# Kernel tuning notes

Hardware: AMD Instinct MI355X
Metric: run time of the kernel (lower is better)

Reference implementation:

```python
import jax, jax.numpy as jnp
import numpy as np

B, S, HID, NH = 2, 2048, 1024, 16
HD = HID // NH
NEG = -1e10


def setup_inputs() -> dict:
    key = jax.random.key(0)
    ks = jax.random.split(key, 14)
    s = 0.02
    return {
        "query": jax.random.normal(ks[0], (B, S, HID), jnp.float32),
        "key_": jax.random.normal(ks[1], (B, S, HID), jnp.float32),
        "value": jax.random.normal(ks[2], (B, S, HID), jnp.float32),
        "mask": jax.random.randint(ks[3], (B, 1, 1, S), 0, 2, jnp.int32),
        "Wq": jax.random.normal(ks[4], (HID, HID), jnp.float32) * s,
        "bq": jnp.zeros((HID,), jnp.float32),
        "Wk": jax.random.normal(ks[5], (HID, HID), jnp.float32) * s,
        "bk": jnp.zeros((HID,), jnp.float32),
        "Wv": jax.random.normal(ks[6], (HID, HID), jnp.float32) * s,
        "bv": jnp.zeros((HID,), jnp.float32),
        "Ww": jax.random.normal(ks[7], (HD, HD), jnp.float32) * s,
        "bw": jnp.zeros((HD,), jnp.float32),
        "Wo": jax.random.normal(ks[8], (HID, HID), jnp.float32) * s,
        "bo": jnp.zeros((HID,), jnp.float32),
    }


def reference(query, key_, value, mask, Wq, bq, Wk, bk, Wv, bv, Ww, bw, Wo, bo):
    def heads(x, W, b):
        h = x @ W.T + b                       # [B,S,HID]
        return h.reshape(B, S, NH, HD).transpose(0, 2, 1, 3)  # [B,H,S,D]

    Q = heads(query, Wq, bq)
    K = heads(key_, Wk, bk)
    V = heads(value, Wv, bv)
    # multiplicative: per-head linear on Q before QK^T (no 1/sqrt(d) scale)
    Qw = Q @ Ww.T + bw                        # [B,H,S,D]
    energy = jnp.einsum('bhqd,bhkd->bhqk', Qw, K)
    energy = jnp.where(mask == 0, jnp.float32(NEG), energy)
    attention = jax.nn.softmax(energy, axis=-1)
    x = jnp.einsum('bhqk,bhkd->bhqd', attention, V)  # dropout p=0 (eval)
    x = x.transpose(0, 2, 1, 3).reshape(B, S, HID)
    x = x @ Wo.T + bo
    return (x, attention)
```

## Files before the change

kernel.cpp:

```cpp
#include <hip/hip_runtime.h>
#include <hip/hip_bf16.h>

#define B_    2
#define S_    2048
#define HID_  1024
#define NH_   16
#define HD_   64
#define M_    (B_ * S_)
#define NEGB_ (-1.0e30f)
#define LOG2E 1.44269504088896340736f
#define X_ELEMS 4194304

typedef __bf16 bf16;
typedef bf16  bf16x2 __attribute__((ext_vector_type(2)));
typedef bf16  bf16x4 __attribute__((ext_vector_type(4)));
typedef bf16  bf16x8 __attribute__((ext_vector_type(8)));
typedef float f32x4  __attribute__((ext_vector_type(4)));

static __device__ __forceinline__ f32x4 mfma16(bf16x8 a, bf16x8 b, f32x4 c) {
    return __builtin_amdgcn_mfma_f32_16x16x32_bf16(a, b, c, 0, 0, 0);
}

static __device__ __forceinline__ int pack2(float x, float y) {
    union { bf16x2 h; int i; } u;
    u.h = bf16x2{(bf16)x, (bf16)y};
    return u.i;
}

static __device__ __forceinline__ int swadr(int row, int chunk) {
    return row * 128 + ((chunk ^ (row & 7)) << 4);
}
static __device__ __forceinline__ bf16x8 lds8(const bf16* base, int row, int chunk) {
    return *(const bf16x8*)((const char*)base + swadr(row, chunk));
}


__global__ void cast3(const float* __restrict__ a, const float* __restrict__ b,
                      const float* __restrict__ c, bf16* __restrict__ oa,
                      bf16* __restrict__ ob, bf16* __restrict__ oc) {
    const float* in = blockIdx.y == 0 ? a : blockIdx.y == 1 ? b : c;
    bf16* out = blockIdx.y == 0 ? oa : blockIdx.y == 1 ? ob : oc;
    int i = (blockIdx.x * 256 + threadIdx.x) * 4;
    float4 v = *(const float4*)(in + i);
    out[i + 0] = (bf16)v.x;
    out[i + 1] = (bf16)v.y;
    out[i + 2] = (bf16)v.z;
    out[i + 3] = (bf16)v.w;
}

__global__ __launch_bounds__(256) void fuse_wq(const float* __restrict__ Ww,
                                               const float* __restrict__ Wq,
                                               const float* __restrict__ bq,
                                               const float* __restrict__ bw,
                                               bf16* __restrict__ Wq_eff,
                                               float* __restrict__ bq_eff) {
    __shared__ float ww[64][64];
    const int h = blockIdx.x >> 2, chunk = blockIdx.x & 3;
    const int i = chunk * 256 + threadIdx.x;
    for (int t = threadIdx.x; t < 4096; t += 256) ww[t >> 6][t & 63] = Ww[t];
    __syncthreads();
    float col[64];
    #pragma unroll
    for (int d = 0; d < 64; ++d) col[d] = Wq[(size_t)(h * 64 + d) * 1024 + i];
    for (int j = 0; j < 64; ++j) {
        float acc = 0.f;
        #pragma unroll
        for (int d = 0; d < 64; ++d) acc += ww[j][d] * col[d];
        Wq_eff[(size_t)(h * 64 + j) * 1024 + i] = (bf16)(acc * LOG2E);
    }
    if (chunk == 0 && threadIdx.x < 64) {
        int j = threadIdx.x;
        float acc = bw[j];
        for (int d = 0; d < 64; ++d) acc += ww[j][d] * bq[h * 64 + d];
        bq_eff[h * 64 + j] = acc * LOG2E;
    }
}

__global__ __launch_bounds__(256, 3) void proj3(const float* __restrict__ Aq,
                                                const float* __restrict__ Ak,
                                                const float* __restrict__ Av,
                                                const bf16* __restrict__ W0,
                                                const bf16* __restrict__ W1,
                                                const bf16* __restrict__ W2,
                                                const float* __restrict__ b0,
                                                const float* __restrict__ b1,
                                                const float* __restrict__ b2,
                                                bf16* __restrict__ Qw,
                                                bf16* __restrict__ Kh,
                                                bf16* __restrict__ Vt) {
    __shared__ __align__(16) bf16 Ast[2][128 * 64];
    __shared__ __align__(16) bf16 Wst[2][64 * 64];
    const int z = blockIdx.z;
    const float* A = z == 0 ? Aq : z == 1 ? Ak : Av;
    const bf16* W = z == 0 ? W0 : z == 1 ? W1 : W2;
    const float* bias = z == 0 ? b0 : z == 1 ? b1 : b2;

    const int tid = threadIdx.x;
    const int wave = tid >> 6, lane = tid & 63;
    const int lr = lane & 15, kg = lane >> 4;
    const int mb0 = blockIdx.x * 128;
    const int n0 = blockIdx.y * 64;

    const int arow = tid >> 1, akc = (tid & 1) * 32;
    const int wrow = tid >> 2, wkc = (tid & 3) * 16;

    float4 ar[8];
    bf16x8 wr[2];
    auto loadT = [&](int k0) {
        const float4* ap = (const float4*)(A + (size_t)(mb0 + arow) * HID_ + k0 + akc);
        #pragma unroll
        for (int j = 0; j < 8; ++j) ar[j] = ap[j];
        const bf16* wp = W + (size_t)(n0 + wrow) * HID_ + k0 + wkc;
        wr[0] = *(const bf16x8*)wp;
        wr[1] = *(const bf16x8*)(wp + 8);
    };
    auto writeT = [&](int buf) {
        #pragma unroll
        for (int c = 0; c < 4; ++c) {
            float4 x0 = ar[2 * c], x1 = ar[2 * c + 1];
            bf16x8 v;
            v[0] = (bf16)x0.x; v[1] = (bf16)x0.y; v[2] = (bf16)x0.z; v[3] = (bf16)x0.w;
            v[4] = (bf16)x1.x; v[5] = (bf16)x1.y; v[6] = (bf16)x1.z; v[7] = (bf16)x1.w;
            *(bf16x8*)((char*)Ast[buf] + swadr(arow, (akc >> 3) + c)) = v;
        }
        *(bf16x8*)((char*)Wst[buf] + swadr(wrow, wkc >> 3)) = wr[0];
        *(bf16x8*)((char*)Wst[buf] + swadr(wrow, (wkc >> 3) + 1)) = wr[1];
    };

    f32x4 acc[2][4] = {};
    loadT(0);
    for (int t = 0; t < 16; ++t) {
        const int buf = t & 1;
        writeT(buf);
        if (t < 15) loadT((t + 1) * 64);
        __syncthreads();
        const bf16* ab = Ast[buf];
        const bf16* wb = Wst[buf];
        #pragma unroll
        for (int kp = 0; kp < 2; ++kp) {
            bf16x8 af0 = lds8(ab, wave * 16 + lr, kp * 4 + kg);
            bf16x8 af1 = lds8(ab, 64 + wave * 16 + lr, kp * 4 + kg);
            #pragma unroll
            for (int nf = 0; nf < 4; ++nf) {
                bf16x8 wf = lds8(wb, nf * 16 + lr, kp * 4 + kg);
                acc[0][nf] = mfma16(af0, wf, acc[0][nf]);
                acc[1][nf] = mfma16(af1, wf, acc[1][nf]);
            }
        }
        __syncthreads();
    }

    const int m_base = mb0 + wave * 16;
    #pragma unroll
    for (int t = 0; t < 2; ++t) {
        #pragma unroll
        for (int cg = 0; cg < 4; ++cg) {
            int col = n0 + cg * 16 + lr;
            float bv = bias[col];
            int h = col >> 6, d = col & 63;
            #pragma unroll
            for (int r = 0; r < 4; ++r) {
                int m = m_base + t * 64 + kg * 4 + r;
                int b = m >> 11, s = m & 2047;
                float val = acc[t][cg][r] + bv;
                if (z == 0)
                    Qw[((size_t)(b * NH_ + h) * S_ + s) * HD_ + d] = (bf16)val;
                else if (z == 1)
                    Kh[((size_t)(b * NH_ + h) * S_ + s) * HD_ + d] = (bf16)val;
                else
                    Vt[((size_t)(b * NH_ + h) * HD_ + d) * S_ + s] = (bf16)val;
            }
        }
    }
}

__global__ __launch_bounds__(512, 4) void attn_kernel(const bf16* __restrict__ Qw,
                                                      const bf16* __restrict__ Kh,
                                                      const bf16* __restrict__ Vt,
                                                      const int* __restrict__ mask,
                                                      float* __restrict__ attn_out,
                                                      bf16* __restrict__ Xh) {
    __shared__ __align__(16) float negf[S_];
    __shared__ __align__(16) bf16 Kst[2][4096];
    __shared__ __align__(16) bf16 Vst[2][4096];

    const int lane = threadIdx.x & 63, wave = threadIdx.x >> 6;
    const int lr = lane & 15, kg = lane >> 4;

    const int wg = blockIdx.x;
    const int flat = (wg & 7) * 64 + (wg >> 3);
    const int qtile = flat & 15;
    const int bh = flat >> 4;
    const int b = bh >> 4, h = bh & 15;
    const int q0 = qtile * 128 + wave * 16;

    const bf16* Qh = Qw + (size_t)bh * S_ * HD_;
    const bf16* Kb = Kh + (size_t)bh * S_ * HD_;
    const bf16* Vb = Vt + (size_t)bh * HD_ * S_;
    const int*  mb = mask + b * S_;
    float* arow = attn_out + (size_t)bh * S_ * S_;

    for (int t = threadIdx.x; t < S_; t += 512)
        negf[t] = mb[t] ? 0.f : NEGB_;

    const int srow = threadIdx.x >> 3;
    const int sch  = threadIdx.x & 7;
    const int sdst = srow * 128 + ((sch ^ (srow & 7)) << 4);

    bf16x8 a0 = *(const bf16x8*)(Qh + (size_t)(q0 + lr) * HD_ + kg * 8);
    bf16x8 a1 = *(const bf16x8*)(Qh + (size_t)(q0 + lr) * HD_ + 32 + kg * 8);

    const int addrA = (lr + (((kg << 1)    ) & 3) * 16) << 2;
    const int addrB = (lr + (((kg << 1) | 1) & 3) * 16) << 2;
    const bool lt2 = kg < 2;

    __syncthreads();

    bf16x8 kreg = *(const bf16x8*)(Kb + (size_t)srow * HD_ + sch * 8);
    bf16x8 vreg = *(const bf16x8*)(Vb + (size_t)srow * S_ + sch * 8);

    float psum = 0.f;
    f32x4 X[4] = {};
    for (int t = 0; t < 32; ++t) {
        const int buf = t & 1;
        *(bf16x8*)((char*)Kst[buf] + sdst) = kreg;
        *(bf16x8*)((char*)Vst[buf] + sdst) = vreg;
        if (t + 1 < 32) {
            kreg = *(const bf16x8*)(Kb + (size_t)((t + 1) * 64 + srow) * HD_ + sch * 8);
            vreg = *(const bf16x8*)(Vb + (size_t)srow * S_ + (t + 1) * 64 + sch * 8);
        }
        __syncthreads();
        const bf16* kb = Kst[buf];
        const bf16* vb = Vst[buf];
        #pragma unroll
        for (int s2 = 0; s2 < 2; ++s2) {
            const int rlo = s2 * 32 + lr, rhi = s2 * 32 + 16 + lr;
            bf16x8 k0a = lds8(kb, rlo, kg);
            bf16x8 k1a = lds8(kb, rlo, 4 + kg);
            bf16x8 k0b = lds8(kb, rhi, kg);
            bf16x8 k1b = lds8(kb, rhi, 4 + kg);
            f32x4 e0 = *(const f32x4*)&negf[t * 64 + s2 * 32 + kg * 4];
            f32x4 e1 = *(const f32x4*)&negf[t * 64 + s2 * 32 + 16 + kg * 4];
            e0 = mfma16(k0a, a0, e0);
            e0 = mfma16(k1a, a1, e0);
            e1 = mfma16(k0b, a0, e1);
            e1 = mfma16(k1b, a1, e1);
            f32x4 p0, p1;
            #pragma unroll
            for (int r = 0; r < 4; ++r) { p0[r] = exp2f(e0[r]); p1[r] = exp2f(e1[r]); }
            psum += (p0[0] + p0[1] + p0[2] + p0[3]) + (p1[0] + p1[1] + p1[2] + p1[3]);
            int q0d = pack2(p0[0], p0[1]);
            int q1d = pack2(p0[2], p0[3]);
            int q2d = pack2(p1[0], p1[1]);
            int q3d = pack2(p1[2], p1[3]);
            int bA0 = __builtin_amdgcn_ds_bpermute(addrA, q0d);
            int bA1 = __builtin_amdgcn_ds_bpermute(addrA, q1d);
            int bA2 = __builtin_amdgcn_ds_bpermute(addrA, q2d);
            int bA3 = __builtin_amdgcn_ds_bpermute(addrA, q3d);
            int bB0 = __builtin_amdgcn_ds_bpermute(addrB, q0d);
            int bB1 = __builtin_amdgcn_ds_bpermute(addrB, q1d);
            int bB2 = __builtin_amdgcn_ds_bpermute(addrB, q2d);
            int bB3 = __builtin_amdgcn_ds_bpermute(addrB, q3d);
            union { int d[4]; bf16x8 v; } pau;
            pau.d[0] = lt2 ? bA0 : bA2;
            pau.d[1] = lt2 ? bA1 : bA3;
            pau.d[2] = lt2 ? bB0 : bB2;
            pau.d[3] = lt2 ? bB1 : bB3;
            #pragma unroll
            for (int ds = 0; ds < 4; ++ds) {
                bf16x8 v = lds8(vb, ds * 16 + lr, s2 * 4 + kg);
                X[ds] = mfma16(v, pau.v, X[ds]);
            }
        }
    }

    psum += __shfl_xor(psum, 16);
    psum += __shfl_xor(psum, 32);
    const float lg2l = __log2f(psum);
    const float linv = 1.0f / psum;

    {
        bf16* xrow = Xh + ((size_t)(b * S_ + q0 + lr)) * HID_ + h * HD_;
        #pragma unroll
        for (int ds = 0; ds < 4; ++ds) {
            bf16x4 xv;
            #pragma unroll
            for (int r = 0; r < 4; ++r) xv[r] = (bf16)(X[ds][r] * linv);
            *(bf16x4*)(xrow + ds * 16 + kg * 4) = xv;
        }
    }

    kreg = *(const bf16x8*)(Kb + (size_t)srow * HD_ + sch * 8);
    for (int t = 0; t < 32; ++t) {
        const int buf = t & 1;
        *(bf16x8*)((char*)Kst[buf] + sdst) = kreg;
        if (t + 1 < 32)
            kreg = *(const bf16x8*)(Kb + (size_t)((t + 1) * 64 + srow) * HD_ + sch * 8);
        __syncthreads();
        const bf16* kb = Kst[buf];
        #pragma unroll
        for (int j = 0; j < 4; ++j) {
            const int row = j * 16 + lr;
            bf16x8 k0 = lds8(kb, row, kg);
            bf16x8 k1 = lds8(kb, row, 4 + kg);
            f32x4 z = *(const f32x4*)&negf[t * 64 + j * 16 + kg * 4];
            z[0] -= lg2l; z[1] -= lg2l; z[2] -= lg2l; z[3] -= lg2l;
            z = mfma16(k0, a0, z);
            z = mfma16(k1, a1, z);
            f32x4 p;
            #pragma unroll
            for (int r = 0; r < 4; ++r) p[r] = exp2f(z[r]);
            *(f32x4*)(arow + (size_t)(q0 + lr) * S_ + t * 64 + j * 16 + kg * 4) = p;
        }
    }
}

__global__ __launch_bounds__(256, 3) void out_gemm(const bf16* __restrict__ X,
                                                   const bf16* __restrict__ Wo,
                                                   const float* __restrict__ bo,
                                                   float* __restrict__ out) {
    __shared__ __align__(16) bf16 Ast[2][128 * 64];
    __shared__ __align__(16) bf16 Wst[2][64 * 64];

    const int tid = threadIdx.x;
    const int wave = tid >> 6, lane = tid & 63;
    const int lr = lane & 15, kg = lane >> 4;
    const int mb0 = blockIdx.x * 128;
    const int n0 = blockIdx.y * 64;

    const int arow = tid >> 1, akc = (tid & 1) * 32;
    const int wrow = tid >> 2, wkc = (tid & 3) * 16;

    bf16x8 ar[4];
    bf16x8 wr[2];
    auto loadT = [&](int k0) {
        const bf16* ap = X + (size_t)(mb0 + arow) * HID_ + k0 + akc;
        #pragma unroll
        for (int j = 0; j < 4; ++j) ar[j] = *(const bf16x8*)(ap + j * 8);
        const bf16* wp = Wo + (size_t)(n0 + wrow) * HID_ + k0 + wkc;
        wr[0] = *(const bf16x8*)wp;
        wr[1] = *(const bf16x8*)(wp + 8);
    };
    auto writeT = [&](int buf) {
        #pragma unroll
        for (int c = 0; c < 4; ++c)
            *(bf16x8*)((char*)Ast[buf] + swadr(arow, (akc >> 3) + c)) = ar[c];
        *(bf16x8*)((char*)Wst[buf] + swadr(wrow, wkc >> 3)) = wr[0];
        *(bf16x8*)((char*)Wst[buf] + swadr(wrow, (wkc >> 3) + 1)) = wr[1];
    };

    f32x4 acc[2][4] = {};
    loadT(0);
    for (int t = 0; t < 16; ++t) {
        const int buf = t & 1;
        writeT(buf);
        if (t < 15) loadT((t + 1) * 64);
        __syncthreads();
        const bf16* ab = Ast[buf];
        const bf16* wb = Wst[buf];
        #pragma unroll
        for (int kp = 0; kp < 2; ++kp) {
            bf16x8 af0 = lds8(ab, wave * 16 + lr, kp * 4 + kg);
            bf16x8 af1 = lds8(ab, 64 + wave * 16 + lr, kp * 4 + kg);
            #pragma unroll
            for (int nf = 0; nf < 4; ++nf) {
                bf16x8 wf = lds8(wb, nf * 16 + lr, kp * 4 + kg);
                acc[0][nf] = mfma16(af0, wf, acc[0][nf]);
                acc[1][nf] = mfma16(af1, wf, acc[1][nf]);
            }
        }
        __syncthreads();
    }

    const int m_base = mb0 + wave * 16;
    #pragma unroll
    for (int t = 0; t < 2; ++t) {
        #pragma unroll
        for (int cg = 0; cg < 4; ++cg) {
            int col = n0 + cg * 16 + lr;
            float bv = bo[col];
            #pragma unroll
            for (int r = 0; r < 4; ++r)
                out[(size_t)(m_base + t * 64 + kg * 4 + r) * HID_ + col] = acc[t][cg][r] + bv;
        }
    }
}

extern "C" void kernel_launch(void* const* d_in, const int* in_sizes, int n_in,
                              void* d_out, int out_size, void* d_ws, size_t ws_size,
                              hipStream_t stream) {
    const float* query = (const float*)d_in[0];
    const float* key_  = (const float*)d_in[1];
    const float* value = (const float*)d_in[2];
    const int*   mask  = (const int*)d_in[3];
    const float* Wq = (const float*)d_in[4];
    const float* bq = (const float*)d_in[5];
    const float* Wk = (const float*)d_in[6];
    const float* bk = (const float*)d_in[7];
    const float* Wv = (const float*)d_in[8];
    const float* bv = (const float*)d_in[9];
    const float* Ww = (const float*)d_in[10];
    const float* bw = (const float*)d_in[11];
    const float* Wo = (const float*)d_in[12];
    const float* bo = (const float*)d_in[13];
    float* out = (float*)d_out;

    char* ws = (char*)d_ws;
    size_t off = 0;
    auto alloc = [&](size_t bytes) {
        void* p = ws + off;
        off += (bytes + 255) & ~(size_t)255;
        return p;
    };
    bf16*  Wq_eff = (bf16*)alloc((size_t)HID_ * HID_ * 2);
    float* bq_eff = (float*)alloc((size_t)HID_ * 4);
    bf16*  Wk_b   = (bf16*)alloc((size_t)HID_ * HID_ * 2);
    bf16*  Wv_b   = (bf16*)alloc((size_t)HID_ * HID_ * 2);
    bf16*  Wo_b   = (bf16*)alloc((size_t)HID_ * HID_ * 2);
    bf16*  Qw     = (bf16*)alloc((size_t)M_ * HID_ * 2);
    bf16*  Kh     = (bf16*)alloc((size_t)M_ * HID_ * 2);
    bf16*  Vt     = (bf16*)alloc((size_t)M_ * HID_ * 2);
    bf16*  Xh     = (bf16*)alloc((size_t)M_ * HID_ * 2);
    (void)ws_size; (void)in_sizes; (void)n_in; (void)out_size;

    dim3 gcast(1024, 3);
    cast3<<<gcast, 256, 0, stream>>>(Wk, Wv, Wo, Wk_b, Wv_b, Wo_b);
    fuse_wq<<<64, 256, 0, stream>>>(Ww, Wq, bq, bw, Wq_eff, bq_eff);

    dim3 gproj(M_ / 128, HID_ / 64, 3);
    proj3<<<gproj, 256, 0, stream>>>(query, key_, value,
                                     Wq_eff, Wk_b, Wv_b,
                                     bq_eff, bk, bv,
                                     Qw, Kh, Vt);

    attn_kernel<<<512, 512, 0, stream>>>(Qw, Kh, Vt, mask, out + X_ELEMS, Xh);

    dim3 gout(M_ / 128, HID_ / 64);
    out_gemm<<<gout, 256, 0, stream>>>(Xh, Wo_b, bo, out);
}
```

Measured before the change: 364.0 us.

## Process two query tiles per wave to reuse K/V fragments, halve block size

Each wave now computes 32 query rows (two 16-row sets) instead of 16, reusing the K and V fragments loaded from LDS for both sets. The block shrinks to 256 threads covering the same 128 query rows, with each thread staging two 16-byte chunks per tile. This cuts LDS reads and barrier cost per MFMA but doubles accumulator registers and reduces wave count, which could lower latency hiding.

```diff
diff --git a/kernel.cpp b/kernel.cpp
--- a/kernel.cpp
+++ b/kernel.cpp
@@ -174,7 +174,7 @@
     }
 }
 
-__global__ __launch_bounds__(512, 4) void attn_kernel(const bf16* __restrict__ Qw,
+__global__ __launch_bounds__(256, 3) void attn_kernel(const bf16* __restrict__ Qw,
                                                       const bf16* __restrict__ Kh,
                                                       const bf16* __restrict__ Vt,
                                                       const int* __restrict__ mask,
@@ -184,7 +184,8 @@
     __shared__ __align__(16) bf16 Kst[2][4096];
     __shared__ __align__(16) bf16 Vst[2][4096];
 
-    const int lane = threadIdx.x & 63, wave = threadIdx.x >> 6;
+    const int tid = threadIdx.x;
+    const int lane = tid & 63, wave = tid >> 6;
     const int lr = lane & 15, kg = lane >> 4;
 
     const int wg = blockIdx.x;
@@ -192,7 +193,7 @@
     const int qtile = flat & 15;
     const int bh = flat >> 4;
     const int b = bh >> 4, h = bh & 15;
-    const int q0 = qtile * 128 + wave * 16;
+    const int q0 = qtile * 128 + wave * 32;
 
     const bf16* Qh = Qw + (size_t)bh * S_ * HD_;
     const bf16* Kb = Kh + (size_t)bh * S_ * HD_;
@@ -200,15 +201,18 @@
     const int*  mb = mask + b * S_;
     float* arow = attn_out + (size_t)bh * S_ * S_;
 
-    for (int t = threadIdx.x; t < S_; t += 512)
+    for (int t = tid; t < S_; t += 256)
         negf[t] = mb[t] ? 0.f : NEGB_;
 
-    const int srow = threadIdx.x >> 3;
-    const int sch  = threadIdx.x & 7;
-    const int sdst = srow * 128 + ((sch ^ (srow & 7)) << 4);
-
-    bf16x8 a0 = *(const bf16x8*)(Qh + (size_t)(q0 + lr) * HD_ + kg * 8);
-    bf16x8 a1 = *(const bf16x8*)(Qh + (size_t)(q0 + lr) * HD_ + 32 + kg * 8);
+    const int srow = tid >> 2;
+    const int sc0  = tid & 3;
+
+    bf16x8 aQ[2][2];
+    #pragma unroll
+    for (int set = 0; set < 2; ++set) {
+        aQ[set][0] = *(const bf16x8*)(Qh + (size_t)(q0 + set * 16 + lr) * HD_ + kg * 8);
+        aQ[set][1] = *(const bf16x8*)(Qh + (size_t)(q0 + set * 16 + lr) * HD_ + 32 + kg * 8);
+    }
 
     const int addrA = (lr + (((kg << 1)    ) & 3) * 16) << 2;
     const int addrB = (lr + (((kg << 1) | 1) & 3) * 16) << 2;
@@ -216,86 +220,114 @@
 
     __syncthreads();
 
-    bf16x8 kreg = *(const bf16x8*)(Kb + (size_t)srow * HD_ + sch * 8);
-    bf16x8 vreg = *(const bf16x8*)(Vb + (size_t)srow * S_ + sch * 8);
-
-    float psum = 0.f;
-    f32x4 X[4] = {};
+    bf16x8 kreg[2], vreg[2];
+    #pragma unroll
+    for (int j = 0; j < 2; ++j) {
+        kreg[j] = *(const bf16x8*)(Kb + (size_t)srow * HD_ + (sc0 + 4 * j) * 8);
+        vreg[j] = *(const bf16x8*)(Vb + (size_t)srow * S_ + (sc0 + 4 * j) * 8);
+    }
+
+    float psum[2] = {0.f, 0.f};
+    f32x4 X[2][4] = {};
     for (int t = 0; t < 32; ++t) {
         const int buf = t & 1;
-        *(bf16x8*)((char*)Kst[buf] + sdst) = kreg;
-        *(bf16x8*)((char*)Vst[buf] + sdst) = vreg;
+        #pragma unroll
+        for (int j = 0; j < 2; ++j) {
+            *(bf16x8*)((char*)Kst[buf] + swadr(srow, sc0 + 4 * j)) = kreg[j];
+            *(bf16x8*)((char*)Vst[buf] + swadr(srow, sc0 + 4 * j)) = vreg[j];
+        }
         if (t + 1 < 32) {
-            kreg = *(const bf16x8*)(Kb + (size_t)((t + 1) * 64 + srow) * HD_ + sch * 8);
-            vreg = *(const bf16x8*)(Vb + (size_t)srow * S_ + (t + 1) * 64 + sch * 8);
+            #pragma unroll
+            for (int j = 0; j < 2; ++j) {
+                kreg[j] = *(const bf16x8*)(Kb + (size_t)((t + 1) * 64 + srow) * HD_ + (sc0 + 4 * j) * 8);
+                vreg[j] = *(const bf16x8*)(Vb + (size_t)srow * S_ + (t + 1) * 64 + (sc0 + 4 * j) * 8);
+            }
         }
         __syncthreads();
         const bf16* kb = Kst[buf];
         const bf16* vb = Vst[buf];
         #pragma unroll
         for (int s2 = 0; s2 < 2; ++s2) {
-            const int rlo = s2 * 32 + lr, rhi = s2 * 32 + 16 + lr;
-            bf16x8 k0a = lds8(kb, rlo, kg);
-            bf16x8 k1a = lds8(kb, rlo, 4 + kg);
-            bf16x8 k0b = lds8(kb, rhi, kg);
-            bf16x8 k1b = lds8(kb, rhi, 4 + kg);
-            f32x4 e0 = *(const f32x4*)&negf[t * 64 + s2 * 32 + kg * 4];
-            f32x4 e1 = *(const f32x4*)&negf[t * 64 + s2 * 32 + 16 + kg * 4];
-            e0 = mfma16(k0a, a0, e0);
-            e0 = mfma16(k1a, a1, e0);
-            e1 = mfma16(k0b, a0, e1);
-            e1 = mfma16(k1b, a1, e1);
-            f32x4 p0, p1;
-            #pragma unroll
-            for (int r = 0; r < 4; ++r) { p0[r] = exp2f(e0[r]); p1[r] = exp2f(e1[r]); }
-            psum += (p0[0] + p0[1] + p0[2] + p0[3]) + (p1[0] + p1[1] + p1[2] + p1[3]);
-            int q0d = pack2(p0[0], p0[1]);
-            int q1d = pack2(p0[2], p0[3]);
-            int q2d = pack2(p1[0], p1[1]);
-            int q3d = pack2(p1[2], p1[3]);
-            int bA0 = __builtin_amdgcn_ds_bpermute(addrA, q0d);
-            int bA1 = __builtin_amdgcn_ds_bpermute(addrA, q1d);
-            int bA2 = __builtin_amdgcn_ds_bpermute(addrA, q2d);
-            int bA3 = __builtin_amdgcn_ds_bpermute(addrA, q3d);
-            int bB0 = __builtin_amdgcn_ds_bpermute(addrB, q0d);
-            int bB1 = __builtin_amdgcn_ds_bpermute(addrB, q1d);
-            int bB2 = __builtin_amdgcn_ds_bpermute(addrB, q2d);
-            int bB3 = __builtin_amdgcn_ds_bpermute(addrB, q3d);
-            union { int d[4]; bf16x8 v; } pau;
-            pau.d[0] = lt2 ? bA0 : bA2;
-            pau.d[1] = lt2 ? bA1 : bA3;
-            pau.d[2] = lt2 ? bB0 : bB2;
-            pau.d[3] = lt2 ? bB1 : bB3;
-            #pragma unroll
-            for (int ds = 0; ds < 4; ++ds) {
-                bf16x8 v = lds8(vb, ds * 16 + lr, s2 * 4 + kg);
-                X[ds] = mfma16(v, pau.v, X[ds]);
-            }
-        }
-    }
-
-    psum += __shfl_xor(psum, 16);
-    psum += __shfl_xor(psum, 32);
-    const float lg2l = __log2f(psum);
-    const float linv = 1.0f / psum;
-
-    {
-        bf16* xrow = Xh + ((size_t)(b * S_ + q0 + lr)) * HID_ + h * HD_;
+            bf16x8 k0a = lds8(kb, s2 * 32 + lr, kg);
+            bf16x8 k1a = lds8(kb, s2 * 32 + lr, 4 + kg);
+            bf16x8 k0b = lds8(kb, s2 * 32 + 16 + lr, kg);
+            bf16x8 k1b = lds8(kb, s2 * 32 + 16 + lr, 4 + kg);
+            f32x4 cin0 = *(const f32x4*)&negf[t * 64 + s2 * 32 + kg * 4];
+            f32x4 cin1 = *(const f32x4*)&negf[t * 64 + s2 * 32 + 16 + kg * 4];
+            bf16x8 vv[4];
+            #pragma unroll
+            for (int ds = 0; ds < 4; ++ds)
+                vv[ds] = lds8(vb, ds * 16 + lr, s2 * 4 + kg);
+            #pragma unroll
+            for (int set = 0; set < 2; ++set) {
+                f32x4 e0 = cin0, e1 = cin1;
+                e0 = mfma16(k0a, aQ[set][0], e0);
+                e0 = mfma16(k1a, aQ[set][1], e0);
+                e1 = mfma16(k0b, aQ[set][0], e1);
+                e1 = mfma16(k1b, aQ[set][1], e1);
+                f32x4 p0, p1;
+                #pragma unroll
+                for (int r = 0; r < 4; ++r) { p0[r] = exp2f(e0[r]); p1[r] = exp2f(e1[r]); }
+                psum[set] += (p0[0] + p0[1] + p0[2] + p0[3]) + (p1[0] + p1[1] + p1[2] + p1[3]);
+                int q0d = pack2(p0[0], p0[1]);
+                int q1d = pack2(p0[2], p0[3]);
+                int q2d = pack2(p1[0], p1[1]);
+                int q3d = pack2(p1[2], p1[3]);
+                int bA0 = __builtin_amdgcn_ds_bpermute(addrA, q0d);
+                int bA1 = __builtin_amdgcn_ds_bpermute(addrA, q1d);
+                int bA2 = __builtin_amdgcn_ds_bpermute(addrA, q2d);
+                int bA3 = __builtin_amdgcn_ds_bpermute(addrA, q3d);
+                int bB0 = __builtin_amdgcn_ds_bpermute(addrB, q0d);
+                int bB1 = __builtin_amdgcn_ds_bpermute(addrB, q1d);
+                int bB2 = __builtin_amdgcn_ds_bpermute(addrB, q2d);
+                int bB3 = __builtin_amdgcn_ds_bpermute(addrB, q3d);
+                union { int d[4]; bf16x8 v; } pau;
+                pau.d[0] = lt2 ? bA0 : bA2;
+                pau.d[1] = lt2 ? bA1 : bA3;
+                pau.d[2] = lt2 ? bB0 : bB2;
+                pau.d[3] = lt2 ? bB1 : bB3;
+                #pragma unroll
+                for (int ds = 0; ds < 4; ++ds)
+                    X[set][ds] = mfma16(vv[ds], pau.v, X[set][ds]);
+            }
+        }
+    }
+
+    float lg2l[2], linv[2];
+    #pragma unroll
+    for (int set = 0; set < 2; ++set) {
+        float s = psum[set];
+        s += __shfl_xor(s, 16);
+        s += __shfl_xor(s, 32);
+        lg2l[set] = __log2f(s);
+        linv[set] = 1.0f / s;
+    }
+
+    #pragma unroll
+    for (int set = 0; set < 2; ++set) {
+        bf16* xrow = Xh + ((size_t)(b * S_ + q0 + set * 16 + lr)) * HID_ + h * HD_;
         #pragma unroll
         for (int ds = 0; ds < 4; ++ds) {
             bf16x4 xv;
             #pragma unroll
-            for (int r = 0; r < 4; ++r) xv[r] = (bf16)(X[ds][r] * linv);
+            for (int r = 0; r < 4; ++r) xv[r] = (bf16)(X[set][ds][r] * linv[set]);
             *(bf16x4*)(xrow + ds * 16 + kg * 4) = xv;
         }
     }
 
-    kreg = *(const bf16x8*)(Kb + (size_t)srow * HD_ + sch * 8);
+    #pragma unroll
+    for (int j = 0; j < 2; ++j)
+        kreg[j] = *(const bf16x8*)(Kb + (size_t)srow * HD_ + (sc0 + 4 * j) * 8);
     for (int t = 0; t < 32; ++t) {
         const int buf = t & 1;
-        *(bf16x8*)((char*)Kst[buf] + sdst) = kreg;
-        if (t + 1 < 32)
-            kreg = *(const bf16x8*)(Kb + (size_t)((t + 1) * 64 + srow) * HD_ + sch * 8);
+        #pragma unroll
+        for (int j = 0; j < 2; ++j)
+            *(bf16x8*)((char*)Kst[buf] + swadr(srow, sc0 + 4 * j)) = kreg[j];
+        if (t + 1 < 32) {
+            #pragma unroll
+            for (int j = 0; j < 2; ++j)
+                kreg[j] = *(const bf16x8*)(Kb + (size_t)((t + 1) * 64 + srow) * HD_ + (sc0 + 4 * j) * 8);
+        }
         __syncthreads();
         const bf16* kb = Kst[buf];
         #pragma unroll
@@ -303,14 +335,19 @@
             const int row = j * 16 + lr;
             bf16x8 k0 = lds8(kb, row, kg);
             bf16x8 k1 = lds8(kb, row, 4 + kg);
-            f32x4 z = *(const f32x4*)&negf[t * 64 + j * 16 + kg * 4];
-            z[0] -= lg2l; z[1] -= lg2l; z[2] -= lg2l; z[3] -= lg2l;
-            z = mfma16(k0, a0, z);
-            z = mfma16(k1, a1, z);
-            f32x4 p;
-            #pragma unroll
-            for (int r = 0; r < 4; ++r) p[r] = exp2f(z[r]);
-            *(f32x4*)(arow + (size_t)(q0 + lr) * S_ + t * 64 + j * 16 + kg * 4) = p;
+            f32x4 nb = *(const f32x4*)&negf[t * 64 + j * 16 + kg * 4];
+            #pragma unroll
+            for (int set = 0; set < 2; ++set) {
+                f32x4 z;
+                #pragma unroll
+                for (int r = 0; r < 4; ++r) z[r] = nb[r] - lg2l[set];
+                z = mfma16(k0, aQ[set][0], z);
+                z = mfma16(k1, aQ[set][1], z);
+                f32x4 p;
+                #pragma unroll
+                for (int r = 0; r < 4; ++r) p[r] = exp2f(z[r]);
+                *(f32x4*)(arow + (size_t)(q0 + set * 16 + lr) * S_ + t * 64 + j * 16 + kg * 4) = p;
+            }
         }
     }
 }
@@ -433,7 +470,7 @@
                                      bq_eff, bk, bv,
                                      Qw, Kh, Vt);
 
-    attn_kernel<<<512, 512, 0, stream>>>(Qw, Kh, Vt, mask, out + X_ELEMS, Xh);
+    attn_kernel<<<512, 256, 0, stream>>>(Qw, Kh, Vt, mask, out + X_ELEMS, Xh);
 
     dim3 gout(M_ / 128, HID_ / 64);
     out_gemm<<<gout, 256, 0, stream>>>(Xh, Wo_b, bo, out);
```

Measured after the change: 366.2 us. About the same (+0.6%).

## Split attention into stats and probability-stream kernels; widen projection N tile

Applied to the files above, without the earlier changes.

The fused attention kernel is split into two launches. The first computes softmax row sums and the PV output and writes the sums to a global buffer. The second recomputes QK^T and streams the normalized probabilities to the attention output. Both use 256-thread blocks over 64-query tiles, so there are 1024 blocks each. Separately, the projection GEMM tile grows from 64 to 128 output columns with occupancy 2, which adds reuse of the A tile at the cost of more registers and LDS. The split trades an extra kernel launch and re-reading Q/K against better overlap and occupancy in each phase.

```diff
diff --git a/kernel.cpp b/kernel.cpp
--- a/kernel.cpp
+++ b/kernel.cpp
@@ -76,7 +76,7 @@
     }
 }
 
-__global__ __launch_bounds__(256, 3) void proj3(const float* __restrict__ Aq,
+__global__ __launch_bounds__(256, 2) void proj3(const float* __restrict__ Aq,
                                                 const float* __restrict__ Ak,
                                                 const float* __restrict__ Av,
                                                 const bf16* __restrict__ W0,
@@ -89,7 +89,7 @@
                                                 bf16* __restrict__ Kh,
                                                 bf16* __restrict__ Vt) {
     __shared__ __align__(16) bf16 Ast[2][128 * 64];
-    __shared__ __align__(16) bf16 Wst[2][64 * 64];
+    __shared__ __align__(16) bf16 Wst[2][128 * 64];
     const int z = blockIdx.z;
     const float* A = z == 0 ? Aq : z == 1 ? Ak : Av;
     const bf16* W = z == 0 ? W0 : z == 1 ? W1 : W2;
@@ -99,20 +99,20 @@
     const int wave = tid >> 6, lane = tid & 63;
     const int lr = lane & 15, kg = lane >> 4;
     const int mb0 = blockIdx.x * 128;
-    const int n0 = blockIdx.y * 64;
+    const int n0 = blockIdx.y * 128;
 
     const int arow = tid >> 1, akc = (tid & 1) * 32;
-    const int wrow = tid >> 2, wkc = (tid & 3) * 16;
+    const int wrow = tid >> 1, wkc = (tid & 1) * 32;
 
     float4 ar[8];
-    bf16x8 wr[2];
+    bf16x8 wr[4];
     auto loadT = [&](int k0) {
         const float4* ap = (const float4*)(A + (size_t)(mb0 + arow) * HID_ + k0 + akc);
         #pragma unroll
         for (int j = 0; j < 8; ++j) ar[j] = ap[j];
         const bf16* wp = W + (size_t)(n0 + wrow) * HID_ + k0 + wkc;
-        wr[0] = *(const bf16x8*)wp;
-        wr[1] = *(const bf16x8*)(wp + 8);
+        #pragma unroll
+        for (int j = 0; j < 4; ++j) wr[j] = *(const bf16x8*)(wp + j * 8);
     };
     auto writeT = [&](int buf) {
         #pragma unroll
@@ -123,11 +123,12 @@
             v[4] = (bf16)x1.x; v[5] = (bf16)x1.y; v[6] = (bf16)x1.z; v[7] = (bf16)x1.w;
             *(bf16x8*)((char*)Ast[buf] + swadr(arow, (akc >> 3) + c)) = v;
         }
-        *(bf16x8*)((char*)Wst[buf] + swadr(wrow, wkc >> 3)) = wr[0];
-        *(bf16x8*)((char*)Wst[buf] + swadr(wrow, (wkc >> 3) + 1)) = wr[1];
+        #pragma unroll
+        for (int c = 0; c < 4; ++c)
+            *(bf16x8*)((char*)Wst[buf] + swadr(wrow, (wkc >> 3) + c)) = wr[c];
     };
 
-    f32x4 acc[2][4] = {};
+    f32x4 acc[2][8] = {};
     loadT(0);
     for (int t = 0; t < 16; ++t) {
         const int buf = t & 1;
@@ -141,7 +142,7 @@
             bf16x8 af0 = lds8(ab, wave * 16 + lr, kp * 4 + kg);
             bf16x8 af1 = lds8(ab, 64 + wave * 16 + lr, kp * 4 + kg);
             #pragma unroll
-            for (int nf = 0; nf < 4; ++nf) {
+            for (int nf = 0; nf < 8; ++nf) {
                 bf16x8 wf = lds8(wb, nf * 16 + lr, kp * 4 + kg);
                 acc[0][nf] = mfma16(af0, wf, acc[0][nf]);
                 acc[1][nf] = mfma16(af1, wf, acc[1][nf]);
@@ -154,7 +155,7 @@
     #pragma unroll
     for (int t = 0; t < 2; ++t) {
         #pragma unroll
-        for (int cg = 0; cg < 4; ++cg) {
+        for (int cg = 0; cg < 8; ++cg) {
             int col = n0 + cg * 16 + lr;
             float bv = bias[col];
             int h = col >> 6, d = col & 63;
@@ -174,38 +175,37 @@
     }
 }
 
-__global__ __launch_bounds__(512, 4) void attn_kernel(const bf16* __restrict__ Qw,
-                                                      const bf16* __restrict__ Kh,
-                                                      const bf16* __restrict__ Vt,
-                                                      const int* __restrict__ mask,
-                                                      float* __restrict__ attn_out,
-                                                      bf16* __restrict__ Xh) {
+__global__ __launch_bounds__(256, 4) void attn_stats(const bf16* __restrict__ Qw,
+                                                     const bf16* __restrict__ Kh,
+                                                     const bf16* __restrict__ Vt,
+                                                     const int* __restrict__ mask,
+                                                     float* __restrict__ lsum_g,
+                                                     bf16* __restrict__ Xh) {
     __shared__ __align__(16) float negf[S_];
     __shared__ __align__(16) bf16 Kst[2][4096];
     __shared__ __align__(16) bf16 Vst[2][4096];
 
-    const int lane = threadIdx.x & 63, wave = threadIdx.x >> 6;
+    const int tid = threadIdx.x;
+    const int lane = tid & 63, wave = tid >> 6;
     const int lr = lane & 15, kg = lane >> 4;
 
     const int wg = blockIdx.x;
-    const int flat = (wg & 7) * 64 + (wg >> 3);
-    const int qtile = flat & 15;
-    const int bh = flat >> 4;
+    const int flat = (wg & 7) * 128 + (wg >> 3);
+    const int qtile = flat & 31;
+    const int bh = flat >> 5;
     const int b = bh >> 4, h = bh & 15;
-    const int q0 = qtile * 128 + wave * 16;
+    const int q0 = qtile * 64 + wave * 16;
 
     const bf16* Qh = Qw + (size_t)bh * S_ * HD_;
     const bf16* Kb = Kh + (size_t)bh * S_ * HD_;
     const bf16* Vb = Vt + (size_t)bh * HD_ * S_;
     const int*  mb = mask + b * S_;
-    float* arow = attn_out + (size_t)bh * S_ * S_;
-
-    for (int t = threadIdx.x; t < S_; t += 512)
+
+    for (int t = tid; t < S_; t += 256)
         negf[t] = mb[t] ? 0.f : NEGB_;
 
-    const int srow = threadIdx.x >> 3;
-    const int sch  = threadIdx.x & 7;
-    const int sdst = srow * 128 + ((sch ^ (srow & 7)) << 4);
+    const int srow = tid >> 2;
+    const int sc0  = tid & 3;
 
     bf16x8 a0 = *(const bf16x8*)(Qh + (size_t)(q0 + lr) * HD_ + kg * 8);
     bf16x8 a1 = *(const bf16x8*)(Qh + (size_t)(q0 + lr) * HD_ + 32 + kg * 8);
@@ -216,18 +216,28 @@
 
     __syncthreads();
 
-    bf16x8 kreg = *(const bf16x8*)(Kb + (size_t)srow * HD_ + sch * 8);
-    bf16x8 vreg = *(const bf16x8*)(Vb + (size_t)srow * S_ + sch * 8);
+    bf16x8 kreg[2], vreg[2];
+    #pragma unroll
+    for (int j = 0; j < 2; ++j) {
+        kreg[j] = *(const bf16x8*)(Kb + (size_t)srow * HD_ + (sc0 + 4 * j) * 8);
+        vreg[j] = *(const bf16x8*)(Vb + (size_t)srow * S_ + (sc0 + 4 * j) * 8);
+    }
 
     float psum = 0.f;
     f32x4 X[4] = {};
     for (int t = 0; t < 32; ++t) {
         const int buf = t & 1;
-        *(bf16x8*)((char*)Kst[buf] + sdst) = kreg;
-        *(bf16x8*)((char*)Vst[buf] + sdst) = vreg;
+        #pragma unroll
+        for (int j = 0; j < 2; ++j) {
+            *(bf16x8*)((char*)Kst[buf] + swadr(srow, sc0 + 4 * j)) = kreg[j];
+            *(bf16x8*)((char*)Vst[buf] + swadr(srow, sc0 + 4 * j)) = vreg[j];
+        }
         if (t + 1 < 32) {
-            kreg = *(const bf16x8*)(Kb + (size_t)((t + 1) * 64 + srow) * HD_ + sch * 8);
-            vreg = *(const bf16x8*)(Vb + (size_t)srow * S_ + (t + 1) * 64 + sch * 8);
+            #pragma unroll
+            for (int j = 0; j < 2; ++j) {
+                kreg[j] = *(const bf16x8*)(Kb + (size_t)((t + 1) * 64 + srow) * HD_ + (sc0 + 4 * j) * 8);
+                vreg[j] = *(const bf16x8*)(Vb + (size_t)srow * S_ + (t + 1) * 64 + (sc0 + 4 * j) * 8);
+            }
         }
         __syncthreads();
         const bf16* kb = Kst[buf];
@@ -276,26 +286,70 @@
 
     psum += __shfl_xor(psum, 16);
     psum += __shfl_xor(psum, 32);
-    const float lg2l = __log2f(psum);
+    if (lane < 16) lsum_g[(size_t)bh * S_ + q0 + lr] = psum;
     const float linv = 1.0f / psum;
 
-    {
-        bf16* xrow = Xh + ((size_t)(b * S_ + q0 + lr)) * HID_ + h * HD_;
-        #pragma unroll
-        for (int ds = 0; ds < 4; ++ds) {
-            bf16x4 xv;
-            #pragma unroll
-            for (int r = 0; r < 4; ++r) xv[r] = (bf16)(X[ds][r] * linv);
-            *(bf16x4*)(xrow + ds * 16 + kg * 4) = xv;
-        }
-    }
-
-    kreg = *(const bf16x8*)(Kb + (size_t)srow * HD_ + sch * 8);
+    bf16* xrow = Xh + ((size_t)(b * S_ + q0 + lr)) * HID_ + h * HD_;
+    #pragma unroll
+    for (int ds = 0; ds < 4; ++ds) {
+        bf16x4 xv;
+        #pragma unroll
+        for (int r = 0; r < 4; ++r) xv[r] = (bf16)(X[ds][r] * linv);
+        *(bf16x4*)(xrow + ds * 16 + kg * 4) = xv;
+    }
+}
+
+__global__ __launch_bounds__(256, 4) void attn_pstream(const bf16* __restrict__ Qw,
+                                                       const bf16* __restrict__ Kh,
+                                                       const int* __restrict__ mask,
+                                                       const float* __restrict__ lsum_g,
+                                                       float* __restrict__ attn_out) {
+    __shared__ __align__(16) float negf[S_];
+    __shared__ __align__(16) bf16 Kst[2][4096];
+
+    const int tid = threadIdx.x;
+    const int lane = tid & 63, wave = tid >> 6;
+    const int lr = lane & 15, kg = lane >> 4;
+
+    const int wg = blockIdx.x;
+    const int flat = (wg & 7) * 128 + (wg >> 3);
+    const int qtile = flat & 31;
+    const int bh = flat >> 5;
+    const int b = bh >> 4;
+    const int q0 = qtile * 64 + wave * 16;
+
+    const bf16* Qh = Qw + (size_t)bh * S_ * HD_;
+    const bf16* Kb = Kh + (size_t)bh * S_ * HD_;
+    const int*  mb = mask + b * S_;
+    float* arow = attn_out + (size_t)bh * S_ * S_;
+
+    for (int t = tid; t < S_; t += 256)
+        negf[t] = mb[t] ? 0.f : NEGB_;
+
+    const int srow = tid >> 2;
+    const int sc0  = tid & 3;
+
+    bf16x8 a0 = *(const bf16x8*)(Qh + (size_t)(q0 + lr) * HD_ + kg * 8);
+    bf16x8 a1 = *(const bf16x8*)(Qh + (size_t)(q0 + lr) * HD_ + 32 + kg * 8);
+    const float lg2l = __log2f(lsum_g[(size_t)bh * S_ + q0 + lr]);
+
+    __syncthreads();
+
+    bf16x8 kreg[2];
+    #pragma unroll
+    for (int j = 0; j < 2; ++j)
+        kreg[j] = *(const bf16x8*)(Kb + (size_t)srow * HD_ + (sc0 + 4 * j) * 8);
+
     for (int t = 0; t < 32; ++t) {
         const int buf = t & 1;
-        *(bf16x8*)((char*)Kst[buf] + sdst) = kreg;
-        if (t + 1 < 32)
-            kreg = *(const bf16x8*)(Kb + (size_t)((t + 1) * 64 + srow) * HD_ + sch * 8);
+        #pragma unroll
+        for (int j = 0; j < 2; ++j)
+            *(bf16x8*)((char*)Kst[buf] + swadr(srow, sc0 + 4 * j)) = kreg[j];
+        if (t + 1 < 32) {
+            #pragma unroll
+            for (int j = 0; j < 2; ++j)
+                kreg[j] = *(const bf16x8*)(Kb + (size_t)((t + 1) * 64 + srow) * HD_ + (sc0 + 4 * j) * 8);
+        }
         __syncthreads();
         const bf16* kb = Kst[buf];
         #pragma unroll
@@ -303,8 +357,10 @@
             const int row = j * 16 + lr;
             bf16x8 k0 = lds8(kb, row, kg);
             bf16x8 k1 = lds8(kb, row, 4 + kg);
-            f32x4 z = *(const f32x4*)&negf[t * 64 + j * 16 + kg * 4];
-            z[0] -= lg2l; z[1] -= lg2l; z[2] -= lg2l; z[3] -= lg2l;
+            f32x4 nb = *(const f32x4*)&negf[t * 64 + j * 16 + kg * 4];
+            f32x4 z;
+            #pragma unroll
+            for (int r = 0; r < 4; ++r) z[r] = nb[r] - lg2l;
             z = mfma16(k0, a0, z);
             z = mfma16(k1, a1, z);
             f32x4 p;
@@ -421,19 +477,21 @@
     bf16*  Kh     = (bf16*)alloc((size_t)M_ * HID_ * 2);
     bf16*  Vt     = (bf16*)alloc((size_t)M_ * HID_ * 2);
     bf16*  Xh     = (bf16*)alloc((size_t)M_ * HID_ * 2);
+    float* lsum_g = (float*)alloc((size_t)B_ * NH_ * S_ * 4);
     (void)ws_size; (void)in_sizes; (void)n_in; (void)out_size;
 
     dim3 gcast(1024, 3);
     cast3<<<gcast, 256, 0, stream>>>(Wk, Wv, Wo, Wk_b, Wv_b, Wo_b);
     fuse_wq<<<64, 256, 0, stream>>>(Ww, Wq, bq, bw, Wq_eff, bq_eff);
 
-    dim3 gproj(M_ / 128, HID_ / 64, 3);
+    dim3 gproj(M_ / 128, HID_ / 128, 3);
     proj3<<<gproj, 256, 0, stream>>>(query, key_, value,
                                      Wq_eff, Wk_b, Wv_b,
                                      bq_eff, bk, bv,
                                      Qw, Kh, Vt);
 
-    attn_kernel<<<512, 512, 0, stream>>>(Qw, Kh, Vt, mask, out + X_ELEMS, Xh);
+    attn_stats<<<1024, 256, 0, stream>>>(Qw, Kh, Vt, mask, lsum_g, Xh);
+    attn_pstream<<<1024, 256, 0, stream>>>(Qw, Kh, mask, lsum_g, out + X_ELEMS);
 
     dim3 gout(M_ / 128, HID_ / 64);
     out_gemm<<<gout, 256, 0, stream>>>(Xh, Wo_b, bo, out);
```

Measured after the change: 356.7 us. -2.0%, faster.
